# Optimization experiments

Hardware: AMD Instinct MI355X
Metric: run time of the kernel (lower is better)

Reference implementation:

```python
import jax, jax.numpy as jnp
import numpy as np

DIM = 768
HEADS = 12
DIM_HEAD = 64
ROPE_BASE = 8192.0
LN_EPS = 1e-5


def setup_inputs() -> dict:
    key = jax.random.key(0)
    k1, k2, k3, k4 = jax.random.split(key, 4)
    B, N = 4, 2048
    x = jax.random.normal(k1, (B, N, DIM), dtype=jnp.float32)
    # 2D (time, pitch) coordinates in [0, 64)
    coords = jax.random.uniform(k2, (B, N, 2), dtype=jnp.float32) * 64.0
    ln_gamma = jnp.ones((DIM,), dtype=jnp.float32)
    ln_beta = jnp.zeros((DIM,), dtype=jnp.float32)
    w_qkv = jax.random.normal(k3, (3 * HEADS * DIM_HEAD, DIM), dtype=jnp.float32) * (DIM ** -0.5)
    w_out = jax.random.normal(k4, (DIM, HEADS * DIM_HEAD), dtype=jnp.float32) * ((HEADS * DIM_HEAD) ** -0.5)
    return {"x": x, "coords": coords, "ln_gamma": ln_gamma, "ln_beta": ln_beta,
            "w_qkv": w_qkv, "w_out": w_out}


def _rotate(t, cos, sin):
    # t: [B,H,N,ad]; cos/sin: [B,1,N,ad//2]
    t1 = t[..., 0::2]
    t2 = t[..., 1::2]
    return jnp.concatenate([t1 * cos - t2 * sin, t1 * sin + t2 * cos], axis=-1)


def _axis_cos_sin(coord, axis_dim):
    # coord: [B,N] -> cos/sin: [B,1,N,axis_dim//2]
    half = axis_dim // 2
    exp = jnp.arange(half, dtype=jnp.float32) / half
    inv_freq = jnp.exp(-exp * jnp.log(jnp.float32(ROPE_BASE)))  # [half]
    freqs = coord[:, :, None] * inv_freq[None, None, :]  # [B,N,half]
    return jnp.cos(freqs)[:, None], jnp.sin(freqs)[:, None]


def reference(x, coords, ln_gamma, ln_beta, w_qkv, w_out):
    B, N, D = x.shape
    scale = DIM_HEAD ** -0.5

    # LayerNorm
    mu = jnp.mean(x, axis=-1, keepdims=True)
    var = jnp.mean((x - mu) ** 2, axis=-1, keepdims=True)
    xn = (x - mu) * jax.lax.rsqrt(var + LN_EPS) * ln_gamma + ln_beta

    # QKV projection: [B,N,3*H*dh]
    qkv = jnp.einsum('bnd,ed->bne', xn, w_qkv)
    q, k, v = jnp.split(qkv, 3, axis=-1)

    def to_heads(t):
        return t.reshape(B, N, HEADS, DIM_HEAD).transpose(0, 2, 1, 3)  # b h n d
    q, k, v = to_heads(q), to_heads(k), to_heads(v)

    # 2D axial RoPE: x-axis on dims [0:dh//2), y-axis on dims [dh//2:dh)
    half = DIM_HEAD // 2
    slices = [(0, (0, half)), (1, (half, DIM_HEAD))]
    for axis_idx, (lo, hi) in slices:
        cos, sin = _axis_cos_sin(coords[..., axis_idx], hi - lo)
        q = jnp.concatenate([q[..., :lo], _rotate(q[..., lo:hi], cos, sin), q[..., hi:]], axis=-1)
        k = jnp.concatenate([k[..., :lo], _rotate(k[..., lo:hi], cos, sin), k[..., hi:]], axis=-1)

    # Attention
    dots = jnp.einsum('bhnd,bhmd->bhnm', q, k) * scale
    attn = jax.nn.softmax(dots, axis=-1)
    out = jnp.einsum('bhnm,bhmd->bhnd', attn, v)
    out = out.transpose(0, 2, 1, 3).reshape(B, N, HEADS * DIM_HEAD)
    return jnp.einsum('bne,de->bnd', out, w_out)
```

## Files before the change

### kernel.cpp

```cpp
#include <hip/hip_runtime.h>

#define B_ 4
#define N_ 2048
#define D_ 768
#define H_ 12
#define DH_ 64
#define ROWS_ (B_*N_)
#define E3_ (3*D_)
#define NCVT_ 1152
#define NLN_  2048

typedef _Float16 f16;
typedef __attribute__((ext_vector_type(8))) _Float16 half8;
typedef __attribute__((ext_vector_type(4))) _Float16 half4;
typedef __attribute__((ext_vector_type(2))) _Float16 half2;
typedef __attribute__((ext_vector_type(4))) float floatx4;

__device__ __forceinline__ void gload_lds16(const void* g, void* lds){
  __builtin_amdgcn_global_load_lds(
      (const __attribute__((address_space(1))) unsigned int*)g,
      (__attribute__((address_space(3))) unsigned int*)lds, 16, 0, 0);
}

__global__ __launch_bounds__(256) void prep_kernel(
    const float* __restrict__ wqkv, f16* __restrict__ W16,
    const float* __restrict__ wout, f16* __restrict__ Wo16,
    const float* __restrict__ x, const float* __restrict__ g,
    const float* __restrict__ be, f16* __restrict__ xn,
    const float* __restrict__ coords, float* __restrict__ T){
  int bx = blockIdx.x, tid = threadIdx.x;
  if (bx < NCVT_){
    const int n8a = E3_*D_/8, n8b = D_*D_/8;
    int i = bx*256 + tid;
    const float* src; f16* dst; int j;
    if (i < n8a){ src = wqkv; dst = W16; j = i; }
    else { j = i - n8a; if (j >= n8b) return; src = wout; dst = Wo16; }
    float4 a = ((const float4*)src)[2*j];
    float4 b = ((const float4*)src)[2*j+1];
    half8 h;
    h[0]=(f16)a.x; h[1]=(f16)a.y; h[2]=(f16)a.z; h[3]=(f16)a.w;
    h[4]=(f16)b.x; h[5]=(f16)b.y; h[6]=(f16)b.z; h[7]=(f16)b.w;
    *(half8*)(dst + (size_t)j*8) = h;
  } else if (bx < NCVT_ + NLN_){
    int w = tid >> 6, lane = tid & 63;
    int row = (bx - NCVT_)*4 + w;
    const float* xr = x + (size_t)row * D_;
    int c = lane*4;
    float4 f0 = *(const float4*)(xr + c);
    float4 f1 = *(const float4*)(xr + c + 256);
    float4 f2 = *(const float4*)(xr + c + 512);
    float s  = (f0.x+f0.y+f0.z+f0.w) + (f1.x+f1.y+f1.z+f1.w) + (f2.x+f2.y+f2.z+f2.w);
    float ss = (f0.x*f0.x+f0.y*f0.y+f0.z*f0.z+f0.w*f0.w)
             + (f1.x*f1.x+f1.y*f1.y+f1.z*f1.z+f1.w*f1.w)
             + (f2.x*f2.x+f2.y*f2.y+f2.z*f2.z+f2.w*f2.w);
    #pragma unroll
    for(int off=1; off<64; off<<=1){
      s  += __shfl_xor(s,  off, 64);
      ss += __shfl_xor(ss, off, 64);
    }
    float mean = s * (1.0f/D_);
    float var  = ss * (1.0f/D_) - mean*mean;
    float rstd = rsqrtf(var + 1e-5f);
    f16* xo = xn + (size_t)row * D_;
    #pragma unroll
    for(int part=0; part<3; ++part){
      float4 v = part==0 ? f0 : (part==1 ? f1 : f2);
      float4 gg = *(const float4*)(g  + c + part*256);
      float4 bb = *(const float4*)(be + c + part*256);
      half4 o;
      o[0] = (f16)((v.x-mean)*rstd*gg.x + bb.x);
      o[1] = (f16)((v.y-mean)*rstd*gg.y + bb.y);
      o[2] = (f16)((v.z-mean)*rstd*gg.z + bb.z);
      o[3] = (f16)((v.w-mean)*rstd*gg.w + bb.w);
      *(half4*)(xo + c + part*256) = o;
    }
  } else {
    int i = (bx - NCVT_ - NLN_)*256 + tid;
    int token = i >> 5, ax = (i >> 4) & 1, m = i & 15;
    float coord = coords[(size_t)token*2 + ax];
    float fr = exp2f((float)m * (-13.0f/16.0f));
    float sn, cs;
    sincosf(coord * fr, &sn, &cs);
    T[(size_t)token*64 + ax*32 + m]      = cs;
    T[(size_t)token*64 + ax*32 + 16 + m] = sn;
  }
}

__global__ __launch_bounds__(256) void qkv_gemm(const f16* __restrict__ A,
    const f16* __restrict__ W, const float* __restrict__ T,
    f16* __restrict__ Q, f16* __restrict__ Kt, f16* __restrict__ VT){
  __shared__ __align__(16) char smem[128*136*2];
  f16* sA = (f16*)smem;
  f16* sB = (f16*)(smem + 16384);
  f16* sT = (f16*)smem;
  int tid = threadIdx.x;
  int w = tid >> 6, lane = tid & 63, quad = lane >> 4, l15 = lane & 15;
  int row0 = blockIdx.y * 128;
  int e0   = blockIdx.x * 128;
  int wr = (w >> 1) * 64, wc = (w & 1) * 64;
  int r8 = lane >> 3;
  int sc16 = ((lane & 7) ^ r8) * 8;
  int sw = l15 & 7;
  floatx4 acc[4][4];
  #pragma unroll
  for(int i=0;i<4;++i)
    #pragma unroll
    for(int j=0;j<4;++j) acc[i][j] = (floatx4){0.f,0.f,0.f,0.f};

  for(int k0=0; k0<D_; k0+=64){
    __syncthreads();
    #pragma unroll
    for(int j=0;j<4;++j){
      int rr = j*32 + w*8 + r8;
      gload_lds16(A + (size_t)(row0+rr)*D_ + k0 + sc16, sA + (j*32 + w*8)*64);
      gload_lds16(W + (size_t)(e0 +rr)*D_ + k0 + sc16, sB + (j*32 + w*8)*64);
    }
    __syncthreads();
    #pragma unroll
    for(int kk=0;kk<2;++kk){
      half8 af[4], bf[4];
      #pragma unroll
      for(int mi=0;mi<4;++mi)
        af[mi] = *(const half8*)&sA[(wr + mi*16 + l15)*64 + (((kk*4 + quad) ^ sw) << 3)];
      #pragma unroll
      for(int ni=0;ni<4;++ni)
        bf[ni] = *(const half8*)&sB[(wc + ni*16 + l15)*64 + (((kk*4 + quad) ^ sw) << 3)];
      #pragma unroll
      for(int mi=0;mi<4;++mi)
        #pragma unroll
        for(int ni=0;ni<4;++ni)
          acc[mi][ni] = __builtin_amdgcn_mfma_f32_16x16x32_f16(af[mi], bf[ni], acc[mi][ni], 0, 0, 0);
    }
  }
  int part = e0 / D_;
  int erel = e0 % D_;
  if (part == 2){
    __syncthreads();
    #pragma unroll
    for(int mi=0;mi<4;++mi){
      int r = wr + mi*16 + quad*4;
      #pragma unroll
      for(int ni=0;ni<4;++ni){
        int c = wc + ni*16 + l15;
        #pragma unroll
        for(int reg=0;reg<4;++reg)
          sT[(size_t)(r+reg)*136 + c] = (f16)acc[mi][ni][reg];
      }
    }
    __syncthreads();
    int colT = tid >> 1;
    int nh   = (tid & 1) * 64;
    int h = erel/64 + (colT >> 6);
    int d = colT & 63;
    int rbase = row0 + nh;
    int b = rbase >> 11, n = rbase & 2047;
    f16 tmp[64];
    #pragma unroll
    for(int j=0;j<64;++j) tmp[j] = sT[(size_t)(nh + j)*136 + colT];
    f16* op = VT + (((size_t)b*H_ + h)*DH_ + d)*N_ + n;
    #pragma unroll
    for(int j=0;j<8;++j) *(half8*)(op + j*8) = *(half8*)&tmp[j*8];
    return;
  }
  __syncthreads();
  #pragma unroll
  for(int mi=0;mi<4;++mi){
    int r = wr + mi*16 + quad*4;
    #pragma unroll
    for(int ni=0;ni<4;++ni){
      int c = wc + ni*16 + l15;
      #pragma unroll
      for(int reg=0;reg<4;++reg)
        sT[(size_t)(r+reg)*136 + c] = (f16)acc[mi][ni][reg];
    }
  }
  __syncthreads();
  int r  = tid >> 1;
  int hh = tid & 1;
  int n_global = row0 + r;
  const float* tt = T + (size_t)n_global*64;
  float tv[64];
  #pragma unroll
  for(int j=0;j<16;++j) *(float4*)&tv[j*4] = *(const float4*)(tt + j*4);
  f16 v[64];
  #pragma unroll
  for(int j=0;j<8;++j) *(half8*)&v[j*8] = *(const half8*)&sT[(size_t)r*136 + hh*64 + j*8];
  f16 o[64];
  #pragma unroll
  for(int ax=0; ax<2; ++ax){
    #pragma unroll
    for(int m=0;m<16;++m){
      float cs = tv[ax*32 + m];
      float sn = tv[ax*32 + 16 + m];
      float t1 = (float)v[ax*32 + 2*m];
      float t2 = (float)v[ax*32 + 2*m + 1];
      o[ax*32 + m]      = (f16)(t1*cs - t2*sn);
      o[ax*32 + 16 + m] = (f16)(t1*sn + t2*cs);
    }
  }
  int h = erel/64 + hh;
  int b = n_global >> 11, n = n_global & 2047;
  f16* dst = (part==0) ? Q : Kt;
  f16* op = dst + (((size_t)b*H_ + h)*N_ + n)*DH_;
  #pragma unroll
  for(int j=0;j<8;++j) *(half8*)(op + j*8) = *(half8*)&o[j*8];
}

__global__ __launch_bounds__(256, 3) void attn_kernel(const f16* __restrict__ Q,
    const f16* __restrict__ K, const f16* __restrict__ VT, f16* __restrict__ AO){
  __shared__ f16 sK[2][64*64];
  __shared__ f16 sV[2][64*64];
  __shared__ f16 sP[4][16*64];
  int bh = blockIdx.y;
  int q0 = blockIdx.x * 128;
  int tid = threadIdx.x;
  int w = tid >> 6, lane = tid & 63, quad = lane >> 4, l15 = lane & 15;
  const f16* Qb = Q  + (size_t)bh*N_*DH_;
  const f16* Ks = K  + (size_t)bh*N_*DH_;
  const f16* Vb = VT + (size_t)bh*DH_*N_;

  int sd = tid >> 2, sc = tid & 3;
  const f16* vp = Vb + (size_t)sd*N_ + sc*16;
  const f16* kp = Ks + (size_t)sd*DH_ + sc*16;
  int sw0 = sd*64 + (((2*sc    ) ^ (sd & 7)) << 3);
  int sw1 = sd*64 + (((2*sc + 1) ^ (sd & 7)) << 3);

  half8 qf0[2], qf1[2];
  #pragma unroll
  for(int s2=0;s2<2;++s2){
    const f16* qrow = Qb + (size_t)(q0 + 32*w + 16*s2 + l15)*DH_ + quad*8;
    qf0[s2] = *(const half8*)(qrow);
    qf1[s2] = *(const half8*)(qrow + 32);
    half8 cs8;
    #pragma unroll
    for(int j=0;j<8;++j) cs8[j] = (f16)0.18033688f;
    qf0[s2] = qf0[s2] * cs8;
    qf1[s2] = qf1[s2] * cs8;
  }

  {
    half8 k0 = *(const half8*)(kp);
    half8 k1 = *(const half8*)(kp + 8);
    half8 g0 = *(const half8*)(vp);
    half8 g1 = *(const half8*)(vp + 8);
    *(half8*)&sK[0][sw0] = k0;  *(half8*)&sK[0][sw1] = k1;
    *(half8*)&sV[0][sw0] = g0;  *(half8*)&sV[0][sw1] = g1;
  }
  kp += 64*DH_;  vp += 64;

  float l_run[2] = {0.0f, 0.0f};
  floatx4 acc[2][4];
  #pragma unroll
  for(int s2=0;s2<2;++s2)
    #pragma unroll
    for(int dt=0;dt<4;++dt) acc[s2][dt] = (floatx4){0.f,0.f,0.f,0.f};
  __syncthreads();

  int sw = l15 & 7;
  f16* Pb = &sP[w][l15*64];

  const floatx4 SINIT = (floatx4){-8.f,-8.f,-8.f,-8.f};

#define ATTN_BODY(CUR, NXT) { \
    half8 nk0 = *(const half8*)(kp);      half8 nk1 = *(const half8*)(kp + 8); \
    half8 ng0 = *(const half8*)(vp);      half8 ng1 = *(const half8*)(vp + 8); \
    kp += 64*DH_;  vp += 64; \
    const f16* sk = &sK[CUR][0]; \
    const f16* sv = &sV[CUR][0]; \
    half8 kf0[4], kf1[4]; \
    _Pragma("unroll") \
    for(int nt=0;nt<4;++nt){ \
      int rr = 16*nt + l15; \
      kf0[nt] = *(const half8*)&sk[rr*64 + ((quad       ^ sw) << 3)]; \
      kf1[nt] = *(const half8*)&sk[rr*64 + (((quad + 4) ^ sw) << 3)]; \
    } \
    floatx4 s_[2][4]; \
    _Pragma("unroll") \
    for(int s2=0;s2<2;++s2) \
      _Pragma("unroll") \
      for(int nt=0; nt<4; ++nt){ \
        floatx4 z = SINIT; \
        z = __builtin_amdgcn_mfma_f32_16x16x32_f16(kf0[nt], qf0[s2], z, 0, 0, 0); \
        z = __builtin_amdgcn_mfma_f32_16x16x32_f16(kf1[nt], qf1[s2], z, 0, 0, 0); \
        s_[s2][nt] = z; \
      } \
    _Pragma("unroll") \
    for(int s2=0;s2<2;++s2){ \
      float r4[4]; \
      _Pragma("unroll") \
      for(int nt=0;nt<4;++nt){ \
        float p0 = __builtin_amdgcn_exp2f(s_[s2][nt][0]); \
        float p1 = __builtin_amdgcn_exp2f(s_[s2][nt][1]); \
        float p2 = __builtin_amdgcn_exp2f(s_[s2][nt][2]); \
        float p3 = __builtin_amdgcn_exp2f(s_[s2][nt][3]); \
        auto lo_ = __builtin_amdgcn_cvt_pkrtz(p0, p1); \
        auto hi_ = __builtin_amdgcn_cvt_pkrtz(p2, p3); \
        half2 lo, hi; \
        __builtin_memcpy(&lo, &lo_, 4);  __builtin_memcpy(&hi, &hi_, 4); \
        half4 h = __builtin_shufflevector(lo, hi, 0, 1, 2, 3); \
        *(half4*)&Pb[(((2*nt + (quad>>1)) ^ sw) << 3) + ((quad & 1) << 2)] = h; \
        r4[nt] = (p0+p1)+(p2+p3); \
      } \
      l_run[s2] += (r4[0]+r4[1])+(r4[2]+r4[3]); \
      half8 pf0 = *(const half8*)&Pb[((quad       ^ sw) << 3)]; \
      half8 pf1 = *(const half8*)&Pb[(((4 + quad) ^ sw) << 3)]; \
      _Pragma("unroll") \
      for(int dt=0;dt<4;++dt){ \
        int rr = 16*dt + l15; \
        half8 v0 = *(const half8*)&sv[rr*64 + ((quad       ^ sw) << 3)]; \
        half8 v1 = *(const half8*)&sv[rr*64 + (((quad + 4) ^ sw) << 3)]; \
        acc[s2][dt] = __builtin_amdgcn_mfma_f32_16x16x32_f16(v0, pf0, acc[s2][dt], 0, 0, 0); \
        acc[s2][dt] = __builtin_amdgcn_mfma_f32_16x16x32_f16(v1, pf1, acc[s2][dt], 0, 0, 0); \
      } \
    } \
    { \
      f16* dk = &sK[NXT][0]; \
      f16* dv = &sV[NXT][0]; \
      *(half8*)&dk[sw0] = nk0;  *(half8*)&dk[sw1] = nk1; \
      *(half8*)&dv[sw0] = ng0;  *(half8*)&dv[sw1] = ng1; \
    } \
    __syncthreads(); \
  }

  #pragma unroll 1
  for(int t=0; t<N_/128; ++t){
    ATTN_BODY(0, 1);
    ATTN_BODY(1, 0);
  }
#undef ATTN_BODY

  int b = bh / H_, h = bh % H_;
  #pragma unroll
  for(int s2=0;s2<2;++s2){
    float l = l_run[s2];
    l += __shfl_xor(l, 16, 64);
    l += __shfl_xor(l, 32, 64);
    float inv = 1.0f / l;
    #pragma unroll
    for(int dt=0;dt<4;++dt){
      half4 h4;
      h4[0]=(f16)(acc[s2][dt][0]*inv); h4[1]=(f16)(acc[s2][dt][1]*inv);
      h4[2]=(f16)(acc[s2][dt][2]*inv); h4[3]=(f16)(acc[s2][dt][3]*inv);
      *(half4*)&Pb[(((2*dt + (quad>>1)) ^ sw) << 3) + ((quad & 1) << 2)] = h4;
    }
    half8 o0 = *(const half8*)&Pb[(((2*quad    ) ^ sw) << 3)];
    half8 o1 = *(const half8*)&Pb[(((2*quad + 1) ^ sw) << 3)];
    f16* op = AO + ((size_t)(b*N_ + q0 + 32*w + 16*s2 + l15))*D_ + h*DH_ + quad*16;
    *(half8*)(op)     = o0;
    *(half8*)(op + 8) = o1;
  }
}

__global__ __launch_bounds__(256) void out_gemm(const f16* __restrict__ A,
    const f16* __restrict__ W, float* __restrict__ C){
  __shared__ f16 sA[128*64];
  __shared__ f16 sB[128*64];
  int tid = threadIdx.x;
  int w = tid >> 6, lane = tid & 63, quad = lane >> 4, l15 = lane & 15;
  int row0 = blockIdx.y * 128;
  int e0   = blockIdx.x * 128;
  int wr = (w >> 1) * 64, wc = (w & 1) * 64;
  int r8 = lane >> 3;
  int sc16 = ((lane & 7) ^ r8) * 8;
  int sw = l15 & 7;
  floatx4 acc[4][4];
  #pragma unroll
  for(int i=0;i<4;++i)
    #pragma unroll
    for(int j=0;j<4;++j) acc[i][j] = (floatx4){0.f,0.f,0.f,0.f};

  for(int k0=0; k0<D_; k0+=64){
    __syncthreads();
    #pragma unroll
    for(int j=0;j<4;++j){
      int rr = j*32 + w*8 + r8;
      gload_lds16(A + (size_t)(row0+rr)*D_ + k0 + sc16, sA + (j*32 + w*8)*64);
      gload_lds16(W + (size_t)(e0 +rr)*D_ + k0 + sc16, sB + (j*32 + w*8)*64);
    }
    __syncthreads();
    #pragma unroll
    for(int kk=0;kk<2;++kk){
      half8 af[4], bf[4];
      #pragma unroll
      for(int mi=0;mi<4;++mi)
        af[mi] = *(const half8*)&sA[(wr + mi*16 + l15)*64 + (((kk*4 + quad) ^ sw) << 3)];
      #pragma unroll
      for(int ni=0;ni<4;++ni)
        bf[ni] = *(const half8*)&sB[(wc + ni*16 + l15)*64 + (((kk*4 + quad) ^ sw) << 3)];
      #pragma unroll
      for(int mi=0;mi<4;++mi)
        #pragma unroll
        for(int ni=0;ni<4;++ni)
          acc[mi][ni] = __builtin_amdgcn_mfma_f32_16x16x32_f16(af[mi], bf[ni], acc[mi][ni], 0, 0, 0);
    }
  }
  #pragma unroll
  for(int ni=0;ni<4;++ni){
    int col = e0 + wc + ni*16 + l15;
    #pragma unroll
    for(int mi=0;mi<4;++mi){
      int rbase = row0 + wr + mi*16 + quad*4;
      #pragma unroll
      for(int reg=0;reg<4;++reg)
        C[(size_t)(rbase+reg)*D_ + col] = acc[mi][ni][reg];
    }
  }
}

extern "C" void kernel_launch(void* const* d_in, const int* in_sizes, int n_in,
                              void* d_out, int out_size, void* d_ws, size_t ws_size,
                              hipStream_t stream) {
  (void)in_sizes; (void)n_in; (void)out_size; (void)ws_size;
  const float* x      = (const float*)d_in[0];
  const float* coords = (const float*)d_in[1];
  const float* g      = (const float*)d_in[2];
  const float* be     = (const float*)d_in[3];
  const float* wqkv   = (const float*)d_in[4];
  const float* wout   = (const float*)d_in[5];
  float* out = (float*)d_out;
  char* ws = (char*)d_ws;
  const size_t SEG = (size_t)ROWS_ * D_ * 2;
  f16* xn  = (f16*)(ws + 0*SEG);
  f16* Q   = (f16*)(ws + 1*SEG);
  f16* K   = (f16*)(ws + 2*SEG);
  f16* VT  = (f16*)(ws + 3*SEG);
  f16* AO  = (f16*)(ws + 4*SEG);
  f16* W16 = (f16*)(ws + 5*SEG);
  f16* Wo16= (f16*)(ws + 5*SEG + (size_t)E3_*D_*2);
  float* T = (float*)AO;

  prep_kernel<<<NCVT_ + NLN_ + 1024, 256, 0, stream>>>(
      wqkv, W16, wout, Wo16, x, g, be, xn, coords, T);
  qkv_gemm   <<<dim3(E3_/128, ROWS_/128), 256, 0, stream>>>(xn, W16, T, Q, K, VT);
  attn_kernel<<<dim3(N_/128, B_*H_), 256, 0, stream>>>(Q, K, VT, AO);
  out_gemm   <<<dim3(D_/128, ROWS_/128), 256, 0, stream>>>(AO, Wo16, out);
}
```

Measured before the change: 245.2 us.

## Swizzle workgroup IDs per XCD and share V fragments across P tiles

Result: faster. 237.0 us (-3.3%).

```diff
diff --git a/kernel.cpp b/kernel.cpp
--- a/kernel.cpp
+++ b/kernel.cpp
@@ -94,9 +94,13 @@
   f16* sB = (f16*)(smem + 16384);
   f16* sT = (f16*)smem;
   int tid = threadIdx.x;
+  int wgid = blockIdx.x;
+  int swz = (wgid & 7) * 144 + (wgid >> 3);
+  int row_t = swz / 18;
+  int e_t   = swz - row_t*18;
+  int row0 = row_t * 128;
+  int e0   = e_t * 128;
   int w = tid >> 6, lane = tid & 63, quad = lane >> 4, l15 = lane & 15;
-  int row0 = blockIdx.y * 128;
-  int e0   = blockIdx.x * 128;
   int wr = (w >> 1) * 64, wc = (w & 1) * 64;
   int r8 = lane >> 3;
   int sc16 = ((lane & 7) ^ r8) * 8;
@@ -210,9 +214,11 @@
     const f16* __restrict__ K, const f16* __restrict__ VT, f16* __restrict__ AO){
   __shared__ f16 sK[2][64*64];
   __shared__ f16 sV[2][64*64];
-  __shared__ f16 sP[4][16*64];
-  int bh = blockIdx.y;
-  int q0 = blockIdx.x * 128;
+  __shared__ f16 sP[4][2][16*64];
+  int wgid = blockIdx.x;
+  int swz = (wgid & 7) * 96 + (wgid >> 3);
+  int bh = swz >> 4;
+  int q0 = (swz & 15) * 128;
   int tid = threadIdx.x;
   int w = tid >> 6, lane = tid & 63, quad = lane >> 4, l15 = lane & 15;
   const f16* Qb = Q  + (size_t)bh*N_*DH_;
@@ -257,7 +263,7 @@
   __syncthreads();
 
   int sw = l15 & 7;
-  f16* Pb = &sP[w][l15*64];
+  f16* Prow[2] = { &sP[w][0][l15*64], &sP[w][1][l15*64] };
 
   const floatx4 SINIT = (floatx4){-8.f,-8.f,-8.f,-8.f};
 
@@ -266,7 +272,6 @@
     half8 ng0 = *(const half8*)(vp);      half8 ng1 = *(const half8*)(vp + 8); \
     kp += 64*DH_;  vp += 64; \
     const f16* sk = &sK[CUR][0]; \
-    const f16* sv = &sV[CUR][0]; \
     half8 kf0[4], kf1[4]; \
     _Pragma("unroll") \
     for(int nt=0;nt<4;++nt){ \
@@ -286,6 +291,7 @@
       } \
     _Pragma("unroll") \
     for(int s2=0;s2<2;++s2){ \
+      f16* Pb = Prow[s2]; \
       float r4[4]; \
       _Pragma("unroll") \
       for(int nt=0;nt<4;++nt){ \
@@ -302,15 +308,22 @@
         r4[nt] = (p0+p1)+(p2+p3); \
       } \
       l_run[s2] += (r4[0]+r4[1])+(r4[2]+r4[3]); \
-      half8 pf0 = *(const half8*)&Pb[((quad       ^ sw) << 3)]; \
-      half8 pf1 = *(const half8*)&Pb[(((4 + quad) ^ sw) << 3)]; \
+    } \
+    { \
+      const f16* sv = &sV[CUR][0]; \
+      half8 pf0a = *(const half8*)&Prow[0][((quad       ^ sw) << 3)]; \
+      half8 pf1a = *(const half8*)&Prow[0][(((4 + quad) ^ sw) << 3)]; \
+      half8 pf0b = *(const half8*)&Prow[1][((quad       ^ sw) << 3)]; \
+      half8 pf1b = *(const half8*)&Prow[1][(((4 + quad) ^ sw) << 3)]; \
       _Pragma("unroll") \
       for(int dt=0;dt<4;++dt){ \
         int rr = 16*dt + l15; \
         half8 v0 = *(const half8*)&sv[rr*64 + ((quad       ^ sw) << 3)]; \
         half8 v1 = *(const half8*)&sv[rr*64 + (((quad + 4) ^ sw) << 3)]; \
-        acc[s2][dt] = __builtin_amdgcn_mfma_f32_16x16x32_f16(v0, pf0, acc[s2][dt], 0, 0, 0); \
-        acc[s2][dt] = __builtin_amdgcn_mfma_f32_16x16x32_f16(v1, pf1, acc[s2][dt], 0, 0, 0); \
+        acc[0][dt] = __builtin_amdgcn_mfma_f32_16x16x32_f16(v0, pf0a, acc[0][dt], 0, 0, 0); \
+        acc[0][dt] = __builtin_amdgcn_mfma_f32_16x16x32_f16(v1, pf1a, acc[0][dt], 0, 0, 0); \
+        acc[1][dt] = __builtin_amdgcn_mfma_f32_16x16x32_f16(v0, pf0b, acc[1][dt], 0, 0, 0); \
+        acc[1][dt] = __builtin_amdgcn_mfma_f32_16x16x32_f16(v1, pf1b, acc[1][dt], 0, 0, 0); \
       } \
     } \
     { \
@@ -336,6 +349,7 @@
     l += __shfl_xor(l, 16, 64);
     l += __shfl_xor(l, 32, 64);
     float inv = 1.0f / l;
+    f16* Pb = Prow[s2];
     #pragma unroll
     for(int dt=0;dt<4;++dt){
       half4 h4;
@@ -356,9 +370,13 @@
   __shared__ f16 sA[128*64];
   __shared__ f16 sB[128*64];
   int tid = threadIdx.x;
+  int wgid = blockIdx.x;
+  int swz = (wgid & 7) * 48 + (wgid >> 3);
+  int row_t = swz / 6;
+  int e_t   = swz - row_t*6;
+  int row0 = row_t * 128;
+  int e0   = e_t * 128;
   int w = tid >> 6, lane = tid & 63, quad = lane >> 4, l15 = lane & 15;
-  int row0 = blockIdx.y * 128;
-  int e0   = blockIdx.x * 128;
   int wr = (w >> 1) * 64, wc = (w & 1) * 64;
   int r8 = lane >> 3;
   int sc16 = ((lane & 7) ^ r8) * 8;
@@ -431,7 +449,7 @@
 
   prep_kernel<<<NCVT_ + NLN_ + 1024, 256, 0, stream>>>(
       wqkv, W16, wout, Wo16, x, g, be, xn, coords, T);
-  qkv_gemm   <<<dim3(E3_/128, ROWS_/128), 256, 0, stream>>>(xn, W16, T, Q, K, VT);
-  attn_kernel<<<dim3(N_/128, B_*H_), 256, 0, stream>>>(Q, K, VT, AO);
-  out_gemm   <<<dim3(D_/128, ROWS_/128), 256, 0, stream>>>(AO, Wo16, out);
-}
+  qkv_gemm   <<<1152, 256, 0, stream>>>(xn, W16, T, Q, K, VT);
+  attn_kernel<<<768, 256, 0, stream>>>(Q, K, VT, AO);
+  out_gemm   <<<384, 256, 0, stream>>>(AO, Wo16, out);
+}
```
